# Kernel tuning notes

Hardware: AMD Instinct MI355X
Metric: run time of the kernel (lower is better)

## Reference

```python
import jax, jax.numpy as jnp
import numpy as np

B, NQ, C, NH, H, W, STRIDE, RPE_HID = 2, 300, 256, 8, 64, 64, 16, 512
HD = C // NH


def setup_inputs() -> dict:
    key = jax.random.key(0)
    ks = jax.random.split(key, 24)
    n = lambda i, shape, s=1.0: jax.random.normal(ks[i], shape, jnp.float32) * s
    return {
        "raw_query": n(0, (B, NQ, C)),
        "query_pos": n(1, (B, NQ, C)),
        "reference_points": jax.random.uniform(ks[2], (B, NQ, 4), jnp.float32),
        "raw_src": n(3, (B, H * W, C)),
        "src_pos_embed": n(4, (B, H * W, C)),
        "input_padding_mask": jnp.zeros((B, H * W), jnp.float32),
        "input_spatial_shapes": jnp.array([[H, W]], jnp.int32),
        # q/k/v/proj linear params (stored as [in, out])
        "Wq": n(5, (C, C), 0.02), "bq": jnp.zeros((C,), jnp.float32),
        "Wk": n(6, (C, C), 0.02), "bk": jnp.zeros((C,), jnp.float32),
        "Wv": n(7, (C, C), 0.02), "bv": jnp.zeros((C,), jnp.float32),
        "Wp": n(8, (C, C), 0.02), "bp": jnp.zeros((C,), jnp.float32),
        # CPB MLPs: Linear(2,512)+ReLU+Linear(512,NH,no bias). Deltas are in pixel
        # units (up to ~W*STRIDE), so use a small first-layer scale.
        "cpb1_w1": n(9, (2, RPE_HID), 1e-3), "cpb1_b1": jnp.zeros((RPE_HID,), jnp.float32),
        "cpb1_w2": n(10, (RPE_HID, NH), 0.01),
        "cpb2_w1": n(11, (2, RPE_HID), 1e-3), "cpb2_b1": jnp.zeros((RPE_HID,), jnp.float32),
        "cpb2_w2": n(12, (RPE_HID, NH), 0.01),
    }


def reference(raw_query, query_pos, reference_points, raw_src, src_pos_embed,
              input_padding_mask, input_spatial_shapes,
              Wq, bq, Wk, bk, Wv, bv, Wp, bp,
              cpb1_w1, cpb1_b1, cpb1_w2, cpb2_w1, cpb2_b1, cpb2_w2):
    h = int(input_spatial_shapes[0, 0])
    w = int(input_spatial_shapes[0, 1])
    Bsz, Nq, Cd = raw_query.shape
    nh = NH
    hd = Cd // nh
    scale = hd ** -0.5
    stride = float(STRIDE)

    # q/k/v projections -> (B, heads, tokens, head_dim)
    q = ((raw_query + query_pos) @ Wq + bq).reshape(Bsz, Nq, nh, hd).transpose(0, 2, 1, 3) * scale
    k = ((raw_src + src_pos_embed) @ Wk + bk).reshape(Bsz, h * w, nh, hd).transpose(0, 2, 1, 3)
    v = (raw_src @ Wv + bv).reshape(Bsz, h * w, nh, hd).transpose(0, 2, 1, 3)

    # boxes (cx,cy,w,h) -> corners (x1,y1,x2,y2), scaled to pixel coords
    ctr, sz = reference_points[..., :2], reference_points[..., 2:]
    ref = jnp.concatenate([ctr - sz / 2, ctr + sz / 2], axis=-1)  # (B,Nq,4)
    ref = ref * jnp.array([w * stride, h * stride, w * stride, h * stride], jnp.float32)

    pos_x = (jnp.arange(w, dtype=jnp.float32) + 0.5) * stride  # linspace(0.5,w-0.5,w)*stride
    pos_y = (jnp.arange(h, dtype=jnp.float32) + 0.5) * stride
    delta_x = ref[:, :, None, 0::2] - pos_x[None, None, :, None]  # (B,Nq,w,2)
    delta_y = ref[:, :, None, 1::2] - pos_y[None, None, :, None]  # (B,Nq,h,2)

    # CPB MLPs -> per-head relative position bias
    rpe_x = jax.nn.relu(delta_x @ cpb1_w1 + cpb1_b1) @ cpb1_w2  # (B,Nq,w,nh)
    rpe_y = jax.nn.relu(delta_y @ cpb2_w1 + cpb2_b1) @ cpb2_w2  # (B,Nq,h,nh)
    rpe = (rpe_x[:, :, None, :, :] + rpe_y[:, :, :, None, :]).reshape(Bsz, Nq, h * w, nh)
    rpe = rpe.transpose(0, 3, 1, 2)  # (B,nh,Nq,HW)

    attn = jnp.einsum('bhqd,bhkd->bhqk', q, k) + rpe
    attn = attn + input_padding_mask[:, None, None, :] * (-100.0)
    fi = jnp.finfo(attn.dtype)
    attn = jnp.clip(attn, fi.min, fi.max)
    attn = jax.nn.softmax(attn, axis=-1)

    x = jnp.einsum('bhqk,bhkd->bhqd', attn, v).transpose(0, 2, 1, 3).reshape(Bsz, Nq, Cd)
    return x @ Wp + bp
```

## Files before the change

### kernel.cpp

```cpp
#include <hip/hip_runtime.h>

#define NQT   300
#define HWT   4096
#define CD    256
#define NHEAD 8
#define HDIM  32

__global__ __launch_bounds__(256) void proj_gemm(
    const float* __restrict__ X, const float* __restrict__ Xpos,
    const float* __restrict__ W, const float* __restrict__ bias,
    float* __restrict__ Out, int M, float scale)
{
    __shared__ float As[16][68];
    __shared__ float Bs[16][64];
    const int t  = threadIdx.x;
    const int m0 = blockIdx.x * 64;
    const int n0 = blockIdx.y * 64;
    const int tx = t & 15, ty = t >> 4;
    const int ar = t >> 2, ac4 = t & 3;

    float acc[4][4] = {};

    for (int k0 = 0; k0 < 256; k0 += 16) {
        float4 av = make_float4(0.f, 0.f, 0.f, 0.f);
        const int gr = m0 + ar;
        if (gr < M) {
            av = *(const float4*)(X + (size_t)gr * 256 + k0 + ac4 * 4);
            if (Xpos) {
                float4 pv = *(const float4*)(Xpos + (size_t)gr * 256 + k0 + ac4 * 4);
                av.x += pv.x; av.y += pv.y; av.z += pv.z; av.w += pv.w;
            }
        }
        float4 bv = *(const float4*)(W + (size_t)(k0 + ty) * 256 + n0 + tx * 4);

        __syncthreads();
        As[ac4 * 4 + 0][ar] = av.x;
        As[ac4 * 4 + 1][ar] = av.y;
        As[ac4 * 4 + 2][ar] = av.z;
        As[ac4 * 4 + 3][ar] = av.w;
        *(float4*)&Bs[ty][tx * 4] = bv;
        __syncthreads();

        #pragma unroll
        for (int k = 0; k < 16; ++k) {
            float4 a4 = *(const float4*)&As[k][ty * 4];
            float4 b4 = *(const float4*)&Bs[k][tx * 4];
            float a[4] = {a4.x, a4.y, a4.z, a4.w};
            float b[4] = {b4.x, b4.y, b4.z, b4.w};
            #pragma unroll
            for (int i = 0; i < 4; ++i)
                #pragma unroll
                for (int j = 0; j < 4; ++j)
                    acc[i][j] = fmaf(a[i], b[j], acc[i][j]);
        }
    }

    float4 bb = *(const float4*)(bias + n0 + tx * 4);
    #pragma unroll
    for (int i = 0; i < 4; ++i) {
        int gr = m0 + ty * 4 + i;
        if (gr < M) {
            float4 o;
            o.x = (acc[i][0] + bb.x) * scale;
            o.y = (acc[i][1] + bb.y) * scale;
            o.z = (acc[i][2] + bb.z) * scale;
            o.w = (acc[i][3] + bb.w) * scale;
            *(float4*)(Out + (size_t)gr * 256 + n0 + tx * 4) = o;
        }
    }
}

__global__ __launch_bounds__(256) void rpe_kernel(
    const float* __restrict__ refpts,
    const float* __restrict__ w1x, const float* __restrict__ b1x, const float* __restrict__ w2x,
    const float* __restrict__ w1y, const float* __restrict__ b1y, const float* __restrict__ w2y,
    float* __restrict__ outx, float* __restrict__ outy)
{
    const int axis = blockIdx.y;
    const int item = blockIdx.x * 256 + threadIdx.x;
    const int bq   = __builtin_amdgcn_readfirstlane(item >> 6);
    const int pos  = item & 63;

    const float* w1 = axis ? w1y : w1x;
    const float* b1 = axis ? b1y : b1x;
    const float* w2 = axis ? w2y : w2x;

    float4 r = *(const float4*)(refpts + (size_t)bq * 4);
    float ctr  = axis ? r.y : r.x;
    float half = (axis ? r.w : r.z) * 0.5f;
    float lo = (ctr - half) * 1024.f;
    float hi = (ctr + half) * 1024.f;
    float p  = ((float)pos + 0.5f) * 16.f;
    float d0 = lo - p, d1 = hi - p;

    float a0 = 0.f, a1 = 0.f, a2 = 0.f, a3 = 0.f;
    float a4 = 0.f, a5 = 0.f, a6 = 0.f, a7 = 0.f;

    #pragma unroll 4
    for (int hid = 0; hid < 512; ++hid) {
        float hv = fmaf(d0, w1[hid], fmaf(d1, w1[512 + hid], b1[hid]));
        hv = fmaxf(hv, 0.f);
        float4 wA = *(const float4*)(w2 + (size_t)hid * 8);
        float4 wB = *(const float4*)(w2 + (size_t)hid * 8 + 4);
        a0 = fmaf(hv, wA.x, a0); a1 = fmaf(hv, wA.y, a1);
        a2 = fmaf(hv, wA.z, a2); a3 = fmaf(hv, wA.w, a3);
        a4 = fmaf(hv, wB.x, a4); a5 = fmaf(hv, wB.y, a5);
        a6 = fmaf(hv, wB.z, a6); a7 = fmaf(hv, wB.w, a7);
    }

    float* op = (axis ? outy : outx) + (size_t)bq * 512 + pos;
    op[0]   = a0; op[64]  = a1; op[128] = a2; op[192] = a3;
    op[256] = a4; op[320] = a5; op[384] = a6; op[448] = a7;
}

#define QT 16
#define TK 128

__global__ __launch_bounds__(256) void attn_kernel(
    const float* __restrict__ Q,
    const float* __restrict__ K,
    const float* __restrict__ V,
    const float* __restrict__ RPX,
    const float* __restrict__ RPY,
    const float* __restrict__ mask,
    float* __restrict__ Xout)
{
    __shared__ float Ks[TK][36];
    __shared__ float VsT[32][132];
    __shared__ float Ps[QT][132];
    __shared__ float Rx[QT][66];
    __shared__ float Ry[QT][66];
    __shared__ float Msk[TK];
    __shared__ float Cf[QT];
    __shared__ float Lv[QT];
    __shared__ float AccR[4][QT * 34];

    const int bh = blockIdx.y;
    const int b  = bh >> 3, h = bh & 7;
    const int q0 = blockIdx.x * QT;
    const int t  = threadIdx.x;
    const int wv = t >> 6, lane = t & 63;

    const int qi1 = t >> 4;
    const int g   = t & 15;
    const int qb = lane >> 4;
    const int db = lane & 15;

    const int qrow  = q0 + qi1;
    const int qrowc = qrow < NQT ? qrow : NQT - 1;
    const float* qp = Q + ((size_t)(b * NQT + qrowc)) * 256 + h * HDIM;
    float4 qreg[8];
    #pragma unroll
    for (int c = 0; c < 8; ++c) qreg[c] = *(const float4*)(qp + c * 4);

    for (int i = t; i < QT * 64; i += 256) {
        int qq = i >> 6, x = i & 63;
        int qr = q0 + qq; if (qr >= NQT) qr = NQT - 1;
        size_t base = ((size_t)(b * NQT + qr) * 8 + h) * 64 + x;
        Rx[qq][x] = RPX[base];
        Ry[qq][x] = RPY[base];
    }

    float m_r = -1e30f, l_r = 0.f;
    float accq[4][2] = {};

    for (int k0 = 0; k0 < HWT; k0 += TK) {
        __syncthreads();

        #pragma unroll
        for (int i = 0; i < 4; ++i) {
            int j  = t + 256 * i;
            int kk = j >> 3, seg = j & 7;
            size_t goff = ((size_t)(b * HWT + k0 + kk)) * 256 + h * HDIM + seg * 4;
            float4 kv = *(const float4*)(K + goff);
            float4 vv = *(const float4*)(V + goff);
            *(float4*)&Ks[kk][seg * 4] = kv;
            VsT[seg * 4 + 0][kk] = vv.x;
            VsT[seg * 4 + 1][kk] = vv.y;
            VsT[seg * 4 + 2][kk] = vv.z;
            VsT[seg * 4 + 3][kk] = vv.w;
        }
        if (t < TK) Msk[t] = mask[(size_t)b * HWT + k0 + t];
        __syncthreads();

        float pbuf[8];
        float tmax = -1e30f;
        #pragma unroll
        for (int u = 0; u < 8; ++u) {
            int kk = g + 16 * u;
            float dot = 0.f;
            #pragma unroll
            for (int c = 0; c < 8; ++c) {
                float4 kv = *(const float4*)&Ks[kk][c * 4];
                dot = fmaf(qreg[c].x, kv.x, dot);
                dot = fmaf(qreg[c].y, kv.y, dot);
                dot = fmaf(qreg[c].z, kv.z, dot);
                dot = fmaf(qreg[c].w, kv.w, dot);
            }
            int kg = k0 + kk;
            float s = dot + Rx[qi1][kg & 63] + Ry[qi1][kg >> 6]
                          + Msk[kk] * (-100.f);
            pbuf[u] = s;
            tmax = fmaxf(tmax, s);
        }
        #pragma unroll
        for (int off = 8; off; off >>= 1)
            tmax = fmaxf(tmax, __shfl_xor(tmax, off));
        float m_new = fmaxf(m_r, tmax);
        float c = __expf(m_r - m_new);
        float psum = 0.f;
        #pragma unroll
        for (int u = 0; u < 8; ++u) {
            float pv = __expf(pbuf[u] - m_new);
            Ps[qi1][g + 16 * u] = pv;
            psum += pv;
        }
        #pragma unroll
        for (int off = 8; off; off >>= 1)
            psum += __shfl_xor(psum, off);
        l_r = l_r * c + psum;
        m_r = m_new;
        if (g == 0) Cf[qi1] = c;
        __syncthreads();

        float cf[4];
        #pragma unroll
        for (int i = 0; i < 4; ++i) cf[i] = Cf[qb * 4 + i];
        #pragma unroll
        for (int i = 0; i < 4; ++i) { accq[i][0] *= cf[i]; accq[i][1] *= cf[i]; }

        const int kbase = wv * 32;
        #pragma unroll
        for (int kq = 0; kq < 32; kq += 4) {
            int kk = kbase + kq;
            float4 v0 = *(const float4*)&VsT[db][kk];
            float4 v1 = *(const float4*)&VsT[db + 16][kk];
            #pragma unroll
            for (int i = 0; i < 4; ++i) {
                float4 pp = *(const float4*)&Ps[qb * 4 + i][kk];
                accq[i][0] = fmaf(pp.x, v0.x, accq[i][0]);
                accq[i][0] = fmaf(pp.y, v0.y, accq[i][0]);
                accq[i][0] = fmaf(pp.z, v0.z, accq[i][0]);
                accq[i][0] = fmaf(pp.w, v0.w, accq[i][0]);
                accq[i][1] = fmaf(pp.x, v1.x, accq[i][1]);
                accq[i][1] = fmaf(pp.y, v1.y, accq[i][1]);
                accq[i][1] = fmaf(pp.z, v1.z, accq[i][1]);
                accq[i][1] = fmaf(pp.w, v1.w, accq[i][1]);
            }
        }
    }

    if (g == 0) Lv[qi1] = l_r;
    #pragma unroll
    for (int i = 0; i < 4; ++i) {
        AccR[wv][(qb * 4 + i) * 34 + db]      = accq[i][0];
        AccR[wv][(qb * 4 + i) * 34 + db + 16] = accq[i][1];
    }
    __syncthreads();

    const int oq = t >> 4, od = (t & 15) * 2;
    float r0 = 0.f, r1 = 0.f;
    #pragma unroll
    for (int w = 0; w < 4; ++w) {
        r0 += AccR[w][oq * 34 + od];
        r1 += AccR[w][oq * 34 + od + 1];
    }
    float inv = 1.f / Lv[oq];
    int qrow2 = q0 + oq;
    if (qrow2 < NQT) {
        float2 o; o.x = r0 * inv; o.y = r1 * inv;
        *(float2*)(Xout + ((size_t)(b * NQT + qrow2)) * 256 + h * HDIM + od) = o;
    }
}

extern "C" void kernel_launch(void* const* d_in, const int* in_sizes, int n_in,
                              void* d_out, int out_size, void* d_ws, size_t ws_size,
                              hipStream_t stream)
{
    (void)in_sizes; (void)n_in; (void)out_size; (void)ws_size;

    const float* raw_query = (const float*)d_in[0];
    const float* query_pos = (const float*)d_in[1];
    const float* refpts    = (const float*)d_in[2];
    const float* raw_src   = (const float*)d_in[3];
    const float* src_pos   = (const float*)d_in[4];
    const float* mask      = (const float*)d_in[5];
    const float* Wq = (const float*)d_in[7];
    const float* bq = (const float*)d_in[8];
    const float* Wk = (const float*)d_in[9];
    const float* bk = (const float*)d_in[10];
    const float* Wv = (const float*)d_in[11];
    const float* bv = (const float*)d_in[12];
    const float* Wp = (const float*)d_in[13];
    const float* bp = (const float*)d_in[14];
    const float* c1w1 = (const float*)d_in[15];
    const float* c1b1 = (const float*)d_in[16];
    const float* c1w2 = (const float*)d_in[17];
    const float* c2w1 = (const float*)d_in[18];
    const float* c2b1 = (const float*)d_in[19];
    const float* c2w2 = (const float*)d_in[20];

    float* ws = (float*)d_ws;
    float* Qf = ws;
    float* Kf = Qf + 153600;
    float* Vf = Kf + 2097152;
    float* RX = Vf + 2097152;
    float* RY = RX + 307200;
    float* Xf = RY + 307200;

    dim3 blk(256);
    const float qscale = 0.17677669529663687f;

    proj_gemm<<<dim3(10, 4),  blk, 0, stream>>>(raw_query, query_pos, Wq, bq, Qf, 600,  qscale);
    proj_gemm<<<dim3(128, 4), blk, 0, stream>>>(raw_src,   src_pos,   Wk, bk, Kf, 8192, 1.f);
    proj_gemm<<<dim3(128, 4), blk, 0, stream>>>(raw_src,   nullptr,   Wv, bv, Vf, 8192, 1.f);
    rpe_kernel<<<dim3(150, 2), blk, 0, stream>>>(refpts, c1w1, c1b1, c1w2, c2w1, c2b1, c2w2, RX, RY);
    attn_kernel<<<dim3(19, 16), blk, 0, stream>>>(Qf, Kf, Vf, RX, RY, mask, Xf);
    proj_gemm<<<dim3(10, 4),  blk, 0, stream>>>(Xf, nullptr, Wp, bp, (float*)d_out, 600, 1.f);
}
```

Measured before the change: 351.4 us.

## Split attention over key ranges with combine pass and enlarge GEMM tiles

Turns the attention kernel into a split-K (flash-decoding style) scheme. The 4096 keys are divided into 8 chunks per block, so the grid grows from 304 to 2432 blocks, and a new combine kernel merges the partial max, sum and accumulator values. Inside a block, each thread now handles two queries and a 4x4 output tile, using an XOR-swizzled V-transpose layout in shared memory to reduce bank conflicts. The projection GEMM moves to 128-row tiles with 8x4 outputs per thread. The costs are an extra kernel launch, a round trip of partial results through global memory, and fewer GEMM blocks for the small 600-row projections.

```diff
diff --git a/kernel.cpp b/kernel.cpp
--- a/kernel.cpp
+++ b/kernel.cpp
@@ -2,70 +2,85 @@
 
 #define NQT   300
 #define HWT   4096
-#define CD    256
 #define NHEAD 8
 #define HDIM  32
+#define QT     16
+#define TK     64
+#define NSPLIT 8
+#define KSPLIT 512
+#define NQB    19
+#define RECSZ  544
 
 __global__ __launch_bounds__(256) void proj_gemm(
     const float* __restrict__ X, const float* __restrict__ Xpos,
     const float* __restrict__ W, const float* __restrict__ bias,
     float* __restrict__ Out, int M, float scale)
 {
-    __shared__ float As[16][68];
+    __shared__ float As[16][132];
     __shared__ float Bs[16][64];
     const int t  = threadIdx.x;
-    const int m0 = blockIdx.x * 64;
+    const int m0 = blockIdx.x * 128;
     const int n0 = blockIdx.y * 64;
-    const int tx = t & 15, ty = t >> 4;
-    const int ar = t >> 2, ac4 = t & 3;
-
-    float acc[4][4] = {};
+    const int rg = t >> 4, cg = t & 15;
+    const int lr = t >> 2, lc = t & 3;
+
+    float acc[8][4] = {};
 
     for (int k0 = 0; k0 < 256; k0 += 16) {
-        float4 av = make_float4(0.f, 0.f, 0.f, 0.f);
-        const int gr = m0 + ar;
-        if (gr < M) {
-            av = *(const float4*)(X + (size_t)gr * 256 + k0 + ac4 * 4);
-            if (Xpos) {
-                float4 pv = *(const float4*)(Xpos + (size_t)gr * 256 + k0 + ac4 * 4);
-                av.x += pv.x; av.y += pv.y; av.z += pv.z; av.w += pv.w;
+        float4 av[2];
+        #pragma unroll
+        for (int i = 0; i < 2; ++i) {
+            const int gr = m0 + lr + 64 * i;
+            if (gr < M) {
+                av[i] = *(const float4*)(X + (size_t)gr * 256 + k0 + lc * 4);
+                if (Xpos) {
+                    float4 pv = *(const float4*)(Xpos + (size_t)gr * 256 + k0 + lc * 4);
+                    av[i].x += pv.x; av[i].y += pv.y; av[i].z += pv.z; av[i].w += pv.w;
+                }
+            } else {
+                av[i] = make_float4(0.f, 0.f, 0.f, 0.f);
             }
         }
-        float4 bv = *(const float4*)(W + (size_t)(k0 + ty) * 256 + n0 + tx * 4);
-
-        __syncthreads();
-        As[ac4 * 4 + 0][ar] = av.x;
-        As[ac4 * 4 + 1][ar] = av.y;
-        As[ac4 * 4 + 2][ar] = av.z;
-        As[ac4 * 4 + 3][ar] = av.w;
-        *(float4*)&Bs[ty][tx * 4] = bv;
+        float4 bv = *(const float4*)(W + (size_t)(k0 + (t >> 4)) * 256 + n0 + (t & 15) * 4);
+
+        __syncthreads();
+        #pragma unroll
+        for (int i = 0; i < 2; ++i) {
+            const int row = lr + 64 * i;
+            As[lc * 4 + 0][row] = av[i].x;
+            As[lc * 4 + 1][row] = av[i].y;
+            As[lc * 4 + 2][row] = av[i].z;
+            As[lc * 4 + 3][row] = av[i].w;
+        }
+        *(float4*)&Bs[t >> 4][(t & 15) * 4] = bv;
         __syncthreads();
 
         #pragma unroll
         for (int k = 0; k < 16; ++k) {
-            float4 a4 = *(const float4*)&As[k][ty * 4];
-            float4 b4 = *(const float4*)&Bs[k][tx * 4];
-            float a[4] = {a4.x, a4.y, a4.z, a4.w};
-            float b[4] = {b4.x, b4.y, b4.z, b4.w};
-            #pragma unroll
-            for (int i = 0; i < 4; ++i)
+            float4 a0 = *(const float4*)&As[k][rg * 8];
+            float4 a1 = *(const float4*)&As[k][rg * 8 + 4];
+            float4 b4 = *(const float4*)&Bs[k][cg * 4];
+            float a[8] = {a0.x, a0.y, a0.z, a0.w, a1.x, a1.y, a1.z, a1.w};
+            float bb[4] = {b4.x, b4.y, b4.z, b4.w};
+            #pragma unroll
+            for (int i = 0; i < 8; ++i)
                 #pragma unroll
                 for (int j = 0; j < 4; ++j)
-                    acc[i][j] = fmaf(a[i], b[j], acc[i][j]);
-        }
-    }
-
-    float4 bb = *(const float4*)(bias + n0 + tx * 4);
-    #pragma unroll
-    for (int i = 0; i < 4; ++i) {
-        int gr = m0 + ty * 4 + i;
+                    acc[i][j] = fmaf(a[i], bb[j], acc[i][j]);
+        }
+    }
+
+    float4 bb = *(const float4*)(bias + n0 + cg * 4);
+    #pragma unroll
+    for (int i = 0; i < 8; ++i) {
+        int gr = m0 + rg * 8 + i;
         if (gr < M) {
             float4 o;
             o.x = (acc[i][0] + bb.x) * scale;
             o.y = (acc[i][1] + bb.y) * scale;
             o.z = (acc[i][2] + bb.z) * scale;
             o.w = (acc[i][3] + bb.w) * scale;
-            *(float4*)(Out + (size_t)gr * 256 + n0 + tx * 4) = o;
+            *(float4*)(Out + (size_t)gr * 256 + n0 + cg * 4) = o;
         }
     }
 }
@@ -113,164 +128,217 @@
     op[256] = a4; op[320] = a5; op[384] = a6; op[448] = a7;
 }
 
-#define QT 16
-#define TK 128
-
-__global__ __launch_bounds__(256) void attn_kernel(
+#define KS_O  0
+#define VST_O 2304
+#define PS_O  4480
+#define RX_O  5568
+#define RY_O  6624
+#define MSK_O 7680
+#define CF_O  7744
+#define SM_TOT 7760
+
+__global__ __launch_bounds__(256, 4) void attn_split(
     const float* __restrict__ Q,
     const float* __restrict__ K,
     const float* __restrict__ V,
     const float* __restrict__ RPX,
     const float* __restrict__ RPY,
     const float* __restrict__ mask,
-    float* __restrict__ Xout)
-{
-    __shared__ float Ks[TK][36];
-    __shared__ float VsT[32][132];
-    __shared__ float Ps[QT][132];
-    __shared__ float Rx[QT][66];
-    __shared__ float Ry[QT][66];
-    __shared__ float Msk[TK];
-    __shared__ float Cf[QT];
-    __shared__ float Lv[QT];
-    __shared__ float AccR[4][QT * 34];
+    float* __restrict__ part)
+{
+    __shared__ float sm[SM_TOT];
 
     const int bh = blockIdx.y;
     const int b  = bh >> 3, h = bh & 7;
-    const int q0 = blockIdx.x * QT;
+    const int qb0 = blockIdx.x;
+    const int q0  = qb0 * QT;
+    const int split = blockIdx.z;
+    const int kbase = split * KSPLIT;
     const int t  = threadIdx.x;
-    const int wv = t >> 6, lane = t & 63;
-
-    const int qi1 = t >> 4;
-    const int g   = t & 15;
-    const int qb = lane >> 4;
-    const int db = lane & 15;
-
-    const int qrow  = q0 + qi1;
-    const int qrowc = qrow < NQT ? qrow : NQT - 1;
-    const float* qp = Q + ((size_t)(b * NQT + qrowc)) * 256 + h * HDIM;
-    float4 qreg[8];
-    #pragma unroll
-    for (int c = 0; c < 8; ++c) qreg[c] = *(const float4*)(qp + c * 4);
+    const int qp = t >> 5;
+    const int kg = t & 31;
+    const int s3 = t >> 5;
+    const int qg = (t >> 3) & 3;
+    const int dg = t & 7;
+
+    float4 qreg[2][8];
+    #pragma unroll
+    for (int j = 0; j < 2; ++j) {
+        int qr = q0 + 2 * qp + j;
+        if (qr >= NQT) qr = NQT - 1;
+        const float* qptr = Q + ((size_t)(b * NQT + qr)) * 256 + h * HDIM;
+        #pragma unroll
+        for (int c = 0; c < 8; ++c) qreg[j][c] = *(const float4*)(qptr + c * 4);
+    }
 
     for (int i = t; i < QT * 64; i += 256) {
         int qq = i >> 6, x = i & 63;
         int qr = q0 + qq; if (qr >= NQT) qr = NQT - 1;
         size_t base = ((size_t)(b * NQT + qr) * 8 + h) * 64 + x;
-        Rx[qq][x] = RPX[base];
-        Ry[qq][x] = RPY[base];
-    }
-
-    float m_r = -1e30f, l_r = 0.f;
-    float accq[4][2] = {};
-
-    for (int k0 = 0; k0 < HWT; k0 += TK) {
-        __syncthreads();
-
-        #pragma unroll
-        for (int i = 0; i < 4; ++i) {
-            int j  = t + 256 * i;
+        sm[RX_O + qq * 66 + x] = RPX[base];
+        sm[RY_O + qq * 66 + x] = RPY[base];
+    }
+
+    float m0r = -1e30f, m1r = -1e30f, l0r = 0.f, l1r = 0.f;
+    float accq[4][4] = {};
+
+    for (int k0 = 0; k0 < KSPLIT; k0 += TK) {
+        __syncthreads();
+
+        #pragma unroll
+        for (int i = 0; i < 2; ++i) {
+            int j = t + 256 * i;
             int kk = j >> 3, seg = j & 7;
-            size_t goff = ((size_t)(b * HWT + k0 + kk)) * 256 + h * HDIM + seg * 4;
+            size_t goff = ((size_t)(b * HWT + kbase + k0 + kk)) * 256 + h * HDIM + seg * 4;
             float4 kv = *(const float4*)(K + goff);
             float4 vv = *(const float4*)(V + goff);
-            *(float4*)&Ks[kk][seg * 4] = kv;
-            VsT[seg * 4 + 0][kk] = vv.x;
-            VsT[seg * 4 + 1][kk] = vv.y;
-            VsT[seg * 4 + 2][kk] = vv.z;
-            VsT[seg * 4 + 3][kk] = vv.w;
-        }
-        if (t < TK) Msk[t] = mask[(size_t)b * HWT + k0 + t];
-        __syncthreads();
-
-        float pbuf[8];
-        float tmax = -1e30f;
-        #pragma unroll
-        for (int u = 0; u < 8; ++u) {
-            int kk = g + 16 * u;
-            float dot = 0.f;
+            *(float4*)&sm[KS_O + kk * 36 + seg * 4] = kv;
+            int cb = ((kk >> 2) ^ (seg & 3)) * 4 + (kk & 3);
+            sm[VST_O + (seg * 4 + 0) * 68 + cb] = vv.x;
+            sm[VST_O + (seg * 4 + 1) * 68 + cb] = vv.y;
+            sm[VST_O + (seg * 4 + 2) * 68 + cb] = vv.z;
+            sm[VST_O + (seg * 4 + 3) * 68 + cb] = vv.w;
+        }
+        if (t < TK) sm[MSK_O + t] = mask[(size_t)b * HWT + kbase + k0 + t];
+        __syncthreads();
+
+        float sv0[2], sv1[2];
+        #pragma unroll
+        for (int i = 0; i < 2; ++i) {
+            const int kk = kg + 32 * i;
+            const float* kp = &sm[KS_O + kk * 36];
+            float d0 = 0.f, d1 = 0.f;
             #pragma unroll
             for (int c = 0; c < 8; ++c) {
-                float4 kv = *(const float4*)&Ks[kk][c * 4];
-                dot = fmaf(qreg[c].x, kv.x, dot);
-                dot = fmaf(qreg[c].y, kv.y, dot);
-                dot = fmaf(qreg[c].z, kv.z, dot);
-                dot = fmaf(qreg[c].w, kv.w, dot);
+                float4 kv = *(const float4*)(kp + c * 4);
+                d0 = fmaf(qreg[0][c].x, kv.x, d0);
+                d0 = fmaf(qreg[0][c].y, kv.y, d0);
+                d0 = fmaf(qreg[0][c].z, kv.z, d0);
+                d0 = fmaf(qreg[0][c].w, kv.w, d0);
+                d1 = fmaf(qreg[1][c].x, kv.x, d1);
+                d1 = fmaf(qreg[1][c].y, kv.y, d1);
+                d1 = fmaf(qreg[1][c].z, kv.z, d1);
+                d1 = fmaf(qreg[1][c].w, kv.w, d1);
             }
-            int kg = k0 + kk;
-            float s = dot + Rx[qi1][kg & 63] + Ry[qi1][kg >> 6]
-                          + Msk[kk] * (-100.f);
-            pbuf[u] = s;
-            tmax = fmaxf(tmax, s);
-        }
-        #pragma unroll
-        for (int off = 8; off; off >>= 1)
-            tmax = fmaxf(tmax, __shfl_xor(tmax, off));
-        float m_new = fmaxf(m_r, tmax);
-        float c = __expf(m_r - m_new);
-        float psum = 0.f;
-        #pragma unroll
-        for (int u = 0; u < 8; ++u) {
-            float pv = __expf(pbuf[u] - m_new);
-            Ps[qi1][g + 16 * u] = pv;
-            psum += pv;
-        }
-        #pragma unroll
-        for (int off = 8; off; off >>= 1)
-            psum += __shfl_xor(psum, off);
-        l_r = l_r * c + psum;
-        m_r = m_new;
-        if (g == 0) Cf[qi1] = c;
+            const int kgl = kbase + k0 + kk;
+            const int xl = kgl & 63, yl = kgl >> 6;
+            const float mk = sm[MSK_O + kk] * (-100.f);
+            sv0[i] = d0 + sm[RX_O + (2 * qp) * 66 + xl] + sm[RY_O + (2 * qp) * 66 + yl] + mk;
+            sv1[i] = d1 + sm[RX_O + (2 * qp + 1) * 66 + xl] + sm[RY_O + (2 * qp + 1) * 66 + yl] + mk;
+        }
+        float t0 = fmaxf(sv0[0], sv0[1]);
+        float t1 = fmaxf(sv1[0], sv1[1]);
+        #pragma unroll
+        for (int off = 16; off; off >>= 1) {
+            t0 = fmaxf(t0, __shfl_xor(t0, off));
+            t1 = fmaxf(t1, __shfl_xor(t1, off));
+        }
+        const float mn0 = fmaxf(m0r, t0), mn1 = fmaxf(m1r, t1);
+        const float c0 = __expf(m0r - mn0), c1 = __expf(m1r - mn1);
+        const float p00 = __expf(sv0[0] - mn0), p01 = __expf(sv0[1] - mn0);
+        const float p10 = __expf(sv1[0] - mn1), p11 = __expf(sv1[1] - mn1);
+        sm[PS_O + (2 * qp) * 68 + kg]          = p00;
+        sm[PS_O + (2 * qp) * 68 + kg + 32]     = p01;
+        sm[PS_O + (2 * qp + 1) * 68 + kg]      = p10;
+        sm[PS_O + (2 * qp + 1) * 68 + kg + 32] = p11;
+        float s0 = p00 + p01, s1 = p10 + p11;
+        #pragma unroll
+        for (int off = 16; off; off >>= 1) {
+            s0 += __shfl_xor(s0, off);
+            s1 += __shfl_xor(s1, off);
+        }
+        l0r = l0r * c0 + s0; l1r = l1r * c1 + s1;
+        m0r = mn0; m1r = mn1;
+        if (kg == 0) { sm[CF_O + 2 * qp] = c0; sm[CF_O + 2 * qp + 1] = c1; }
         __syncthreads();
 
         float cf[4];
         #pragma unroll
-        for (int i = 0; i < 4; ++i) cf[i] = Cf[qb * 4 + i];
-        #pragma unroll
-        for (int i = 0; i < 4; ++i) { accq[i][0] *= cf[i]; accq[i][1] *= cf[i]; }
-
-        const int kbase = wv * 32;
-        #pragma unroll
-        for (int kq = 0; kq < 32; kq += 4) {
-            int kk = kbase + kq;
-            float4 v0 = *(const float4*)&VsT[db][kk];
-            float4 v1 = *(const float4*)&VsT[db + 16][kk];
-            #pragma unroll
-            for (int i = 0; i < 4; ++i) {
-                float4 pp = *(const float4*)&Ps[qb * 4 + i][kk];
-                accq[i][0] = fmaf(pp.x, v0.x, accq[i][0]);
-                accq[i][0] = fmaf(pp.y, v0.y, accq[i][0]);
-                accq[i][0] = fmaf(pp.z, v0.z, accq[i][0]);
-                accq[i][0] = fmaf(pp.w, v0.w, accq[i][0]);
-                accq[i][1] = fmaf(pp.x, v1.x, accq[i][1]);
-                accq[i][1] = fmaf(pp.y, v1.y, accq[i][1]);
-                accq[i][1] = fmaf(pp.z, v1.z, accq[i][1]);
-                accq[i][1] = fmaf(pp.w, v1.w, accq[i][1]);
-            }
-        }
-    }
-
-    if (g == 0) Lv[qi1] = l_r;
-    #pragma unroll
-    for (int i = 0; i < 4; ++i) {
-        AccR[wv][(qb * 4 + i) * 34 + db]      = accq[i][0];
-        AccR[wv][(qb * 4 + i) * 34 + db + 16] = accq[i][1];
+        for (int i = 0; i < 4; ++i) cf[i] = sm[CF_O + qg * 4 + i];
+        #pragma unroll
+        for (int i = 0; i < 4; ++i)
+            #pragma unroll
+            for (int d = 0; d < 4; ++d) accq[i][d] *= cf[i];
+
+        const int ks0 = s3 * 8;
+        #pragma unroll
+        for (int kc = 0; kc < 8; kc += 4) {
+            const int kk = ks0 + kc;
+            float4 pv[4], vv[4];
+            #pragma unroll
+            for (int i = 0; i < 4; ++i)
+                pv[i] = *(const float4*)&sm[PS_O + (qg * 4 + i) * 68 + kk];
+            const int p4 = ((kk >> 2) ^ (dg & 3)) * 4;
+            #pragma unroll
+            for (int d = 0; d < 4; ++d)
+                vv[d] = *(const float4*)&sm[VST_O + (dg * 4 + d) * 68 + p4];
+            #pragma unroll
+            for (int i = 0; i < 4; ++i)
+                #pragma unroll
+                for (int d = 0; d < 4; ++d) {
+                    accq[i][d] = fmaf(pv[i].x, vv[d].x, accq[i][d]);
+                    accq[i][d] = fmaf(pv[i].y, vv[d].y, accq[i][d]);
+                    accq[i][d] = fmaf(pv[i].z, vv[d].z, accq[i][d]);
+                    accq[i][d] = fmaf(pv[i].w, vv[d].w, accq[i][d]);
+                }
+        }
+    }
+
+    const size_t rec = ((size_t)(bh * NQB + qb0) * NSPLIT + split) * RECSZ;
+    if (kg == 0) {
+        part[rec + 2 * qp]      = m0r;
+        part[rec + 2 * qp + 1]  = m1r;
+        part[rec + 16 + 2 * qp]     = l0r;
+        part[rec + 16 + 2 * qp + 1] = l1r;
     }
     __syncthreads();
 
-    const int oq = t >> 4, od = (t & 15) * 2;
-    float r0 = 0.f, r1 = 0.f;
-    #pragma unroll
-    for (int w = 0; w < 4; ++w) {
-        r0 += AccR[w][oq * 34 + od];
-        r1 += AccR[w][oq * 34 + od + 1];
-    }
-    float inv = 1.f / Lv[oq];
-    int qrow2 = q0 + oq;
-    if (qrow2 < NQT) {
-        float2 o; o.x = r0 * inv; o.y = r1 * inv;
-        *(float2*)(Xout + ((size_t)(b * NQT + qrow2)) * 256 + h * HDIM + od) = o;
-    }
+    #pragma unroll
+    for (int i = 0; i < 4; ++i)
+        *(float4*)&sm[s3 * 576 + (qg * 4 + i) * 36 + dg * 4] =
+            make_float4(accq[i][0], accq[i][1], accq[i][2], accq[i][3]);
+    __syncthreads();
+
+    {
+        const int q = t >> 4, d2 = (t & 15) * 2;
+        float r0 = 0.f, r1 = 0.f;
+        #pragma unroll
+        for (int s = 0; s < 8; ++s) {
+            r0 += sm[s * 576 + q * 36 + d2];
+            r1 += sm[s * 576 + q * 36 + d2 + 1];
+        }
+        *(float2*)&part[rec + 32 + q * 32 + d2] = make_float2(r0, r1);
+    }
+}
+
+__global__ __launch_bounds__(256) void attn_combine(
+    const float* __restrict__ part, float* __restrict__ Xout)
+{
+    const int gi  = blockIdx.x * 256 + threadIdx.x;
+    const int d   = gi & 31;
+    const int row = gi >> 5;
+    const int bh  = row / NQT;
+    const int q   = row - bh * NQT;
+    const int qblk = q >> 4, qi = q & 15;
+    const float* rp = part + ((size_t)(bh * NQB + qblk) * NSPLIT) * RECSZ;
+
+    float mv[NSPLIT], lv[NSPLIT];
+    float M = -1e30f;
+    #pragma unroll
+    for (int s = 0; s < NSPLIT; ++s) {
+        mv[s] = rp[s * RECSZ + qi];
+        lv[s] = rp[s * RECSZ + 16 + qi];
+        M = fmaxf(M, mv[s]);
+    }
+    float num = 0.f, den = 0.f;
+    #pragma unroll
+    for (int s = 0; s < NSPLIT; ++s) {
+        float w = __expf(mv[s] - M);
+        den = fmaf(w, lv[s], den);
+        num = fmaf(w, rp[s * RECSZ + 32 + qi * 32 + d], num);
+    }
+    const int b = bh >> 3, h = bh & 7;
+    Xout[((size_t)(b * NQT + q)) * 256 + h * HDIM + d] = num / den;
 }
 
 extern "C" void kernel_launch(void* const* d_in, const int* in_sizes, int n_in,
@@ -301,20 +369,22 @@
     const float* c2w2 = (const float*)d_in[20];
 
     float* ws = (float*)d_ws;
-    float* Qf = ws;
-    float* Kf = Qf + 153600;
-    float* Vf = Kf + 2097152;
-    float* RX = Vf + 2097152;
-    float* RY = RX + 307200;
-    float* Xf = RY + 307200;
+    float* Qf   = ws;
+    float* Kf   = Qf + 153600;
+    float* Vf   = Kf + 2097152;
+    float* RX   = Vf + 2097152;
+    float* RY   = RX + 307200;
+    float* Xf   = RY + 307200;
+    float* PART = Xf + 153600;
 
     dim3 blk(256);
     const float qscale = 0.17677669529663687f;
 
-    proj_gemm<<<dim3(10, 4),  blk, 0, stream>>>(raw_query, query_pos, Wq, bq, Qf, 600,  qscale);
-    proj_gemm<<<dim3(128, 4), blk, 0, stream>>>(raw_src,   src_pos,   Wk, bk, Kf, 8192, 1.f);
-    proj_gemm<<<dim3(128, 4), blk, 0, stream>>>(raw_src,   nullptr,   Wv, bv, Vf, 8192, 1.f);
+    proj_gemm<<<dim3(5, 4),  blk, 0, stream>>>(raw_query, query_pos, Wq, bq, Qf, 600,  qscale);
+    proj_gemm<<<dim3(64, 4), blk, 0, stream>>>(raw_src,   src_pos,   Wk, bk, Kf, 8192, 1.f);
+    proj_gemm<<<dim3(64, 4), blk, 0, stream>>>(raw_src,   nullptr,   Wv, bv, Vf, 8192, 1.f);
     rpe_kernel<<<dim3(150, 2), blk, 0, stream>>>(refpts, c1w1, c1b1, c1w2, c2w1, c2b1, c2w2, RX, RY);
-    attn_kernel<<<dim3(19, 16), blk, 0, stream>>>(Qf, Kf, Vf, RX, RY, mask, Xf);
-    proj_gemm<<<dim3(10, 4),  blk, 0, stream>>>(Xf, nullptr, Wp, bp, (float*)d_out, 600, 1.f);
-}
+    attn_split<<<dim3(NQB, 16, NSPLIT), blk, 0, stream>>>(Qf, Kf, Vf, RX, RY, mask, PART);
+    attn_combine<<<dim3(600), blk, 0, stream>>>(PART, Xf);
+    proj_gemm<<<dim3(5, 4),  blk, 0, stream>>>(Xf, nullptr, Wp, bp, (float*)d_out, 600, 1.f);
+}
```

New measurement: 492.4 us. 1.4x slower.
